# Kernel optimization log

Measured on AMD Instinct MI355X. Metric: run time of the kernel, lower is better.

## Reference

```python
import jax, jax.numpy as jnp
import numpy as np

# Skeleton structure (start, end) connections
REAL_CONNECTIONS = [(0,1),(1,2),(2,3),(3,4),(1,5),(5,6),(6,7),(7,8),(8,9),(8,13),(8,17),(8,21),(8,25),(9,10),(10,11),(11,12),(13,14),(14,15),(15,16),(17,18),(18,19),(19,20),(21,22),(22,23),(23,24),(25,26),(26,27),(27,28),(4,29),(29,30),(29,34),(29,38),(29,42),(29,46),(30,31),(31,32),(32,33),(34,35),(35,36),(36,37),(38,39),(39,40),(40,41),(42,43),(43,44),(44,45),(46,47),(47,48),(48,49)]

def _bone_ranges():
    # dict insertion order matters only for iteration; result is a sum so order-free
    ranges = {(0,1):(0.05,0.15),(1,2):(0.1,0.2),(1,5):(0.1,0.2),(2,3):(0.2,0.35),(3,4):(0.2,0.35),(5,6):(0.2,0.35),(6,7):(0.2,0.35),(4,8):(0.05,0.15),(7,29):(0.05,0.15)}
    for s, e in REAL_CONNECTIONS:
        if 8 <= s < 50 and 8 <= e < 50:
            ranges[(s, e)] = (0.01, 0.08)
    return ranges

_BR = _bone_ranges()
BONE_S = np.array([k[0] for k in _BR], np.int32)
BONE_E = np.array([k[1] for k in _BR], np.int32)
BONE_MIN = np.array([v[0] for v in _BR.values()], np.float32)
BONE_MAX = np.array([v[1] for v in _BR.values()], np.float32)

SYM_L = np.array([8 + i for i in range(21)] + [2, 3, 4], np.int32)
SYM_R = np.array([29 + i for i in range(21)] + [5, 6, 7], np.int32)

ANG_A = np.array([1, 1, 2, 5], np.int32)
ANG_B = np.array([2, 5, 3, 6], np.int32)
ANG_C = np.array([3, 6, 4, 7], np.int32)

CONN_S = np.array([c[0] for c in REAL_CONNECTIONS], np.int32)
CONN_E = np.array([c[1] for c in REAL_CONNECTIONS], np.int32)

DEG = np.float32(180.0 / np.pi)
EPS = np.float32(1e-12)

def _relu(x):
    return jnp.maximum(x, 0.0)

def _normalize(v):
    n = jnp.linalg.norm(v, axis=-1, keepdims=True)
    return v / jnp.maximum(n, EPS)

def setup_inputs() -> dict:
    key = jax.random.key(0)
    k1, k2 = jax.random.split(key)
    B, S, D = 64, 2048, 150
    pred_poses = jax.random.normal(k1, (B, S, D), dtype=jnp.float32)
    target_poses = jax.random.normal(k2, (B, S, D), dtype=jnp.float32)
    return {"pred_poses": pred_poses, "target_poses": target_poses}

def reference(pred_poses, target_poses):
    B, S, _ = pred_poses.shape
    J = pred_poses.reshape(B, S, 50, 3)
    T = target_poses.reshape(B, S, 50, 3)

    # ---- bone length loss (49 constrained bones, one gathered pass) ----
    bv = J[:, :, BONE_E] - J[:, :, BONE_S]                 # [B,S,49,3]
    bl = jnp.linalg.norm(bv, axis=-1)                      # [B,S,49]
    bone_pen = _relu(bl - BONE_MAX) + _relu(BONE_MIN - bl)
    bone_loss = bone_pen.mean()  # == sum over bones of per-bone mean / n_bones

    # ---- joint angle loss (4 triples) ----
    v1 = _normalize(J[:, :, ANG_A] - J[:, :, ANG_B])       # [B,S,4,3]
    v2 = _normalize(J[:, :, ANG_C] - J[:, :, ANG_B])
    cos = jnp.clip(jnp.sum(v1 * v2, axis=-1), -1.0, 1.0)
    deg = jnp.arccos(cos) * DEG
    angle_loss = (_relu(30.0 - deg) + _relu(deg - 150.0)).mean()

    # ---- symmetry loss (24 pairs) ----
    L = J[:, :, SYM_L]                                     # [B,S,24,3]
    R = J[:, :, SYM_R]
    x_sym = jnp.abs(L[..., 0] + R[..., 0])                 # [B,S,24]
    yz_sim = jnp.abs(L[..., 1:] - R[..., 1:]).mean(axis=-1)
    symmetry_loss = (x_sym + yz_sim).mean()

    # ---- temporal consistency ----
    vel = J[:, 1:] - J[:, :-1]                             # [B,S-1,50,3]
    acc = vel[:, 1:] - vel[:, :-1]
    temporal_loss = jnp.linalg.norm(acc, axis=-1).mean() + 0.5 * jnp.linalg.norm(vel, axis=-1).mean()

    # ---- supervised bone-length consistency (all 49 connections) ----
    tb = jnp.linalg.norm(T[:, :, CONN_E] - T[:, :, CONN_S], axis=-1)
    pb = jnp.linalg.norm(J[:, :, CONN_E] - J[:, :, CONN_S], axis=-1)
    supervised_loss = jnp.abs(pb - tb).mean()

    total = (1.0 * bone_loss + 0.5 * angle_loss + 0.3 * symmetry_loss
             + 0.2 * temporal_loss + supervised_loss)
    return bone_loss, angle_loss, symmetry_loss, temporal_loss, supervised_loss, total
```

## Files before the change

kernel.cpp:

```cpp
#include <hip/hip_runtime.h>
#include <math.h>

#define TPB 256
#define CH  16
#define CPB 8

static constexpr int B_     = 64;
static constexpr int S_     = 2048;
static constexpr int TOTAL  = B_ * S_;
static constexpr int NCHUNK = TOTAL / CH;
static constexpr int NBLK   = NCHUNK / CPB;
static constexpr int SAMPB  = 600;
static constexpr int PREDB  = (CH + 2) * SAMPB;
static constexpr int TGTB   = CH * SAMPB;
static constexpr int CHB    = PREDB + TGTB;
static constexpr int BUFB   = 20480;
static constexpr long TOTB  = (long)TOTAL * SAMPB;

__constant__ int US_[51] = {0,1,1,2,3,5,6,4,7,7,4,
    8,8,8,8,8,9,10,11,13,14,
    15,17,18,19,21,22,23,25,26,27,
    29,29,29,29,29,30,31,32,34,35,
    36,38,39,40,42,43,44,46,47,48};
__constant__ int UE_[51] = {1,2,5,3,4,6,7,8,29,8,29,
    9,13,17,21,25,10,11,12,14,15,
    16,18,19,20,22,23,24,26,27,28,
    30,34,38,42,46,31,32,33,35,36,
    37,39,40,41,43,44,45,47,48,49};
__constant__ float UMIN11_[11] = {0.05f,0.1f,0.1f,0.2f,0.2f,0.2f,0.2f,0.05f,0.05f,-1e9f,-1e9f};
__constant__ float UMAX11_[11] = {0.15f,0.2f,0.2f,0.35f,0.35f,0.35f,0.35f,0.15f,0.15f,1e9f,1e9f};
__constant__ float WSUP11_[11] = {1.f,1.f,1.f,1.f,1.f,1.f,1.f,0.f,0.f,1.f,1.f};
__constant__ int SL_[24] = {8,9,10,11,12,13,14,15,16,17,18,19,20,21,22,23,24,25,26,27,28,2,3,4};
__constant__ int SR_[24] = {29,30,31,32,33,34,35,36,37,38,39,40,41,42,43,44,45,46,47,48,49,5,6,7};
__constant__ int AJ_[4] = {1,1,2,5};
__constant__ int BJ_[4] = {2,5,3,6};
__constant__ int CJ_[4] = {3,6,4,7};

struct F3 { float x, y, z; };
__device__ __forceinline__ F3 ld3(const float* p) { return *(const F3*)p; }

typedef const __attribute__((address_space(1))) void* gas_t;
typedef __attribute__((address_space(3))) void* las_t;

__global__ __launch_bounds__(TPB, 4) void pose_main(
    const float* __restrict__ pred, const float* __restrict__ tgt,
    float* __restrict__ part)
{
    __shared__ __align__(16) char LDS[2 * BUFB];

    const int tid = threadIdx.x;
    const int blk = blockIdx.x;
    const int li  = tid & 15;
    const int g   = tid >> 4;
    const int jb  = li * 150;

    int   uS[3], uE[3];
    float uMn[3], uMx[3], uW[3];
    #pragma unroll
    for (int s = 0; s < 3; ++s) {
        const int k = g + 16 * s;
        uS[s] = jb + US_[k] * 3;  uE[s] = jb + UE_[k] * 3;
        uMn[s] = (k < 11) ? UMIN11_[k] : 0.01f;
        uMx[s] = (k < 11) ? UMAX11_[k] : 0.08f;
        uW[s]  = (k < 11) ? WSUP11_[k] : 1.f;
    }
    const int t3 = g - 12;
    const int ke = 48 + (t3 < 0 ? 0 : (t3 > 2 ? 2 : t3));
    const bool e_on = (g >= 12 && g < 15);
    const int   eS = jb + US_[ke] * 3, eE = jb + UE_[ke] * 3;
    const float eMn = e_on ? 0.01f : -1e9f;
    const float eMx = e_on ? 0.08f :  1e9f;
    const float eW  = e_on ? 1.f   :  0.f;
    const int s0L = jb + SL_[g] * 3, s0R = jb + SR_[g] * 3;
    const int k1  = 16 + ((g - 4) & 7);
    const int s1L = jb + SL_[k1] * 3, s1R = jb + SR_[k1] * 3;
    const int aA = jb + AJ_[g & 3] * 3, aB = jb + BJ_[g & 3] * 3, aC = jb + CJ_[g & 3] * 3;
    const int tb0 = jb + 3 * g;
    const int jx  = 48 + ((g - 4) & 1);
    const int tbx = jb + 3 * (jx > 49 ? 49 : jx);
    const bool tex_on = (g == 4 || g == 5);

    float a_bone = 0.f, a_ang = 0.f, a_sym = 0.f, a_vel = 0.f, a_acc = 0.f, a_sup = 0.f;

    auto stage = [&](int cidx, char* lbuf) {
        const long nb = (long)cidx * TGTB;
        const char* pb = (const char*)pred + nb;
        const char* tb = (const char*)tgt  + nb - PREDB;
        const long prem = TOTB - nb - 16;
        char* wdst = lbuf + ((tid >> 6) << 10);
        #pragma unroll
        for (int s = 0; s < 5; ++s) {
            const long o = (long)tid * 16 + s * 4096;
            const char* src = (o < PREDB)
                ? pb + (o > prem ? prem : o)
                : tb + (o > (long)(CHB - 16) ? (long)(CHB - 16) : o);
            __builtin_amdgcn_global_load_lds((gas_t)src, (las_t)(wdst + s * 4096), 16, 0, 0);
        }
    };

    const int c0 = blk * CPB;
    stage(c0, LDS);

    #pragma unroll
    for (int c = 0; c < CPB; ++c) {
        char* curb = LDS + (c & 1) * BUFB;
        char* nxtb = LDS + ((c & 1) ^ 1) * BUFB;
        if (c + 1 < CPB) {
            stage(c0 + c + 1, nxtb);
            asm volatile("s_waitcnt vmcnt(5)" ::: "memory");
        } else {
            asm volatile("s_waitcnt vmcnt(0)" ::: "memory");
        }
        __builtin_amdgcn_s_barrier();
        __builtin_amdgcn_sched_barrier(0);

        const float* Jl = (const float*)curb;
        const float* Tl = Jl + PREDB / 4;
        const int cidx = c0 + c;

        #pragma unroll
        for (int s = 0; s < 3; ++s) {
            const F3 je = ld3(Jl + uE[s]), js = ld3(Jl + uS[s]);
            const float dx = je.x - js.x, dy = je.y - js.y, dz = je.z - js.z;
            const float pb = sqrtf(dx * dx + dy * dy + dz * dz);
            a_bone += fmaxf(pb - uMx[s], 0.f) + fmaxf(uMn[s] - pb, 0.f);
            const F3 te = ld3(Tl + uE[s]), ts = ld3(Tl + uS[s]);
            const float tx = te.x - ts.x, ty = te.y - ts.y, tz = te.z - ts.z;
            const float tb = sqrtf(tx * tx + ty * ty + tz * tz);
            a_sup += uW[s] * fabsf(pb - tb);
        }
        if (tid >= 192) {
            const F3 je = ld3(Jl + eE), js = ld3(Jl + eS);
            const float dx = je.x - js.x, dy = je.y - js.y, dz = je.z - js.z;
            const float pb = sqrtf(dx * dx + dy * dy + dz * dz);
            a_bone += fmaxf(pb - eMx, 0.f) + fmaxf(eMn - pb, 0.f);
            const F3 te = ld3(Tl + eE), ts = ld3(Tl + eS);
            const float tx = te.x - ts.x, ty = te.y - ts.y, tz = te.z - ts.z;
            const float tb = sqrtf(tx * tx + ty * ty + tz * tz);
            a_sup += eW * fabsf(pb - tb);
        }

        {
            const F3 L = ld3(Jl + s0L), R = ld3(Jl + s0R);
            a_sym += fabsf(L.x + R.x) + 0.5f * (fabsf(L.y - R.y) + fabsf(L.z - R.z));
        }
        if (tid >= 64 && tid < 192) {
            const F3 L = ld3(Jl + s1L), R = ld3(Jl + s1R);
            a_sym += fabsf(L.x + R.x) + 0.5f * (fabsf(L.y - R.y) + fabsf(L.z - R.z));
        }

        if (tid < 64) {
            const F3 A = ld3(Jl + aA), Bb = ld3(Jl + aB), C = ld3(Jl + aC);
            const float v1x = A.x - Bb.x, v1y = A.y - Bb.y, v1z = A.z - Bb.z;
            const float v2x = C.x - Bb.x, v2y = C.y - Bb.y, v2z = C.z - Bb.z;
            const float n12 = (v1x*v1x + v1y*v1y + v1z*v1z) * (v2x*v2x + v2y*v2y + v2z*v2z);
            const float inv = __frsqrt_rn(fmaxf(n12, 1e-24f));
            float cosv = (v1x*v2x + v1y*v2y + v1z*v2z) * inv;
            cosv = fminf(fmaxf(cosv, -1.f), 1.f);
            const float deg = acosf(cosv) * 57.29577951308232f;
            a_ang += fmaxf(30.f - deg, 0.f) + fmaxf(deg - 150.f, 0.f);
        }

        {
            const int sidx = ((cidx * CH) & (S_ - 1)) + li;
            const bool v_ok = sidx < S_ - 1;
            const bool a_ok = sidx < S_ - 2;
            const float* tp = Jl + tb0;
            #pragma unroll
            for (int s = 0; s < 3; ++s) {
                const F3 p0 = ld3(tp + 48*s), p1 = ld3(tp + 48*s + 150), p2 = ld3(tp + 48*s + 300);
                if (v_ok) {
                    const float vx = p1.x - p0.x, vy = p1.y - p0.y, vz = p1.z - p0.z;
                    a_vel += sqrtf(vx*vx + vy*vy + vz*vz);
                    if (a_ok) {
                        const float ax = p2.x - 2.f*p1.x + p0.x;
                        const float ay = p2.y - 2.f*p1.y + p0.y;
                        const float az = p2.z - 2.f*p1.z + p0.z;
                        a_acc += sqrtf(ax*ax + ay*ay + az*az);
                    }
                }
            }
            if (tid >= 64 && tid < 128) {
                const float* tq = Jl + tbx;
                const F3 p0 = ld3(tq), p1 = ld3(tq + 150), p2 = ld3(tq + 300);
                if (tex_on && v_ok) {
                    const float vx = p1.x - p0.x, vy = p1.y - p0.y, vz = p1.z - p0.z;
                    a_vel += sqrtf(vx*vx + vy*vy + vz*vz);
                    if (a_ok) {
                        const float ax = p2.x - 2.f*p1.x + p0.x;
                        const float ay = p2.y - 2.f*p1.y + p0.y;
                        const float az = p2.z - 2.f*p1.z + p0.z;
                        a_acc += sqrtf(ax*ax + ay*ay + az*az);
                    }
                }
            }
        }

        asm volatile("" ::: "memory");
        __builtin_amdgcn_s_barrier();
    }

    float vals[6] = {a_bone, a_ang, a_sym, a_vel, a_acc, a_sup};
    #pragma unroll
    for (int k = 0; k < 6; ++k)
        #pragma unroll
        for (int off = 32; off > 0; off >>= 1)
            vals[k] += __shfl_down(vals[k], off, 64);

    float* red = (float*)LDS;
    const int wid = tid >> 6, lane = tid & 63;
    if (lane == 0) {
        #pragma unroll
        for (int k = 0; k < 6; ++k) red[wid * 6 + k] = vals[k];
    }
    __syncthreads();
    if (tid == 0) {
        #pragma unroll
        for (int k = 0; k < 6; ++k)
            part[k * NBLK + blk] = red[k] + red[6 + k] + red[12 + k] + red[18 + k];
    }
}

__global__ __launch_bounds__(256) void pose_reduce(
    const float* __restrict__ part, float* __restrict__ out)
{
    __shared__ float red[4][6];
    const int tid = threadIdx.x;
    float a[6];
    #pragma unroll
    for (int k = 0; k < 6; ++k) {
        float s = 0.f;
        for (int i = tid; i < NBLK; i += 256) s += part[k * NBLK + i];
        a[k] = s;
    }
    #pragma unroll
    for (int k = 0; k < 6; ++k)
        #pragma unroll
        for (int off = 32; off > 0; off >>= 1)
            a[k] += __shfl_down(a[k], off, 64);

    const int wid = tid >> 6, lane = tid & 63;
    if (lane == 0) {
        #pragma unroll
        for (int k = 0; k < 6; ++k) red[wid][k] = a[k];
    }
    __syncthreads();
    if (tid == 0) {
        float t[6];
        #pragma unroll
        for (int k = 0; k < 6; ++k) t[k] = red[0][k] + red[1][k] + red[2][k] + red[3][k];
        const float bone = t[0] * (1.f / ((float)TOTAL * 49.f));
        const float ang  = t[1] * (1.f / ((float)TOTAL * 4.f));
        const float sym  = t[2] * (1.f / ((float)TOTAL * 24.f));
        const float temporal = t[4] * (1.f / ((float)B_ * (float)(S_ - 2) * 50.f))
                             + 0.5f * t[3] * (1.f / ((float)B_ * (float)(S_ - 1) * 50.f));
        const float sup  = t[5] * (1.f / ((float)TOTAL * 49.f));
        out[0] = bone;
        out[1] = ang;
        out[2] = sym;
        out[3] = temporal;
        out[4] = sup;
        out[5] = bone + 0.5f * ang + 0.3f * sym + 0.2f * temporal + sup;
    }
}

extern "C" void kernel_launch(void* const* d_in, const int* in_sizes, int n_in,
                              void* d_out, int out_size, void* d_ws, size_t ws_size,
                              hipStream_t stream)
{
    const float* pred = (const float*)d_in[0];
    const float* tgt  = (const float*)d_in[1];
    float* part = (float*)d_ws;
    pose_main<<<NBLK, TPB, 0, stream>>>(pred, tgt, part);
    pose_reduce<<<1, 256, 0, stream>>>(part, (float*)d_out);
}
```

Baseline: 43.78 us.

## Double block size to 512 threads and redistribute per-thread work

Raises the block to 512 threads (8 waves). Each thread now handles about one bone, symmetry pair and temporal joint instead of up to three, and the staging loads are spread across 8 waves. The per-wave waitcnt values are adjusted to match the uneven load counts. The goal is shorter per-thread serial chains and more latency hiding, at the cost of more idle lanes and heavier barrier synchronisation per block.

```diff
diff --git a/kernel.cpp b/kernel.cpp
--- a/kernel.cpp
+++ b/kernel.cpp
@@ -1,7 +1,7 @@
 #include <hip/hip_runtime.h>
 #include <math.h>
 
-#define TPB 256
+#define TPB 512
 #define CH  16
 #define CPB 8
 
@@ -42,7 +42,7 @@
 typedef const __attribute__((address_space(1))) void* gas_t;
 typedef __attribute__((address_space(3))) void* las_t;
 
-__global__ __launch_bounds__(TPB, 4) void pose_main(
+__global__ __launch_bounds__(TPB, 8) void pose_main(
     const float* __restrict__ pred, const float* __restrict__ tgt,
     float* __restrict__ part)
 {
@@ -54,47 +54,39 @@
     const int g   = tid >> 4;
     const int jb  = li * 150;
 
-    int   uS[3], uE[3];
-    float uMn[3], uMx[3], uW[3];
-    #pragma unroll
-    for (int s = 0; s < 3; ++s) {
-        const int k = g + 16 * s;
-        uS[s] = jb + US_[k] * 3;  uE[s] = jb + UE_[k] * 3;
-        uMn[s] = (k < 11) ? UMIN11_[k] : 0.01f;
-        uMx[s] = (k < 11) ? UMAX11_[k] : 0.08f;
-        uW[s]  = (k < 11) ? WSUP11_[k] : 1.f;
-    }
-    const int t3 = g - 12;
-    const int ke = 48 + (t3 < 0 ? 0 : (t3 > 2 ? 2 : t3));
-    const bool e_on = (g >= 12 && g < 15);
-    const int   eS = jb + US_[ke] * 3, eE = jb + UE_[ke] * 3;
-    const float eMn = e_on ? 0.01f : -1e9f;
-    const float eMx = e_on ? 0.08f :  1e9f;
-    const float eW  = e_on ? 1.f   :  0.f;
-    const int s0L = jb + SL_[g] * 3, s0R = jb + SR_[g] * 3;
-    const int k1  = 16 + ((g - 4) & 7);
-    const int s1L = jb + SL_[k1] * 3, s1R = jb + SR_[k1] * 3;
+    const int   uS0 = jb + US_[g] * 3, uE0 = jb + UE_[g] * 3;
+    const float uMn0 = (g < 11) ? UMIN11_[g] : 0.01f;
+    const float uMx0 = (g < 11) ? UMAX11_[g] : 0.08f;
+    const float uW0  = (g < 11) ? WSUP11_[g] : 1.f;
+    const bool u1_on = (g < 19);
+    const int  k1u   = u1_on ? g + 32 : 50;
+    const int  uS1 = jb + US_[k1u] * 3, uE1 = jb + UE_[k1u] * 3;
+    const bool sy_on = (g < 24);
+    const int  ks  = sy_on ? g : 0;
+    const int  s0L = jb + SL_[ks] * 3, s0R = jb + SR_[ks] * 3;
     const int aA = jb + AJ_[g & 3] * 3, aB = jb + BJ_[g & 3] * 3, aC = jb + CJ_[g & 3] * 3;
-    const int tb0 = jb + 3 * g;
-    const int jx  = 48 + ((g - 4) & 1);
-    const int tbx = jb + 3 * (jx > 49 ? 49 : jx);
-    const bool tex_on = (g == 4 || g == 5);
+    const int  tb0 = jb + 3 * g;
+    const bool t1_on = (g < 18);
 
     float a_bone = 0.f, a_ang = 0.f, a_sym = 0.f, a_vel = 0.f, a_acc = 0.f, a_sup = 0.f;
 
+    const int w      = tid >> 6;
+    const int lane16 = (tid & 63) << 4;
     auto stage = [&](int cidx, char* lbuf) {
         const long nb = (long)cidx * TGTB;
         const char* pb = (const char*)pred + nb;
         const char* tb = (const char*)tgt  + nb - PREDB;
         const long prem = TOTB - nb - 16;
-        char* wdst = lbuf + ((tid >> 6) << 10);
-        #pragma unroll
-        for (int s = 0; s < 5; ++s) {
-            const long o = (long)tid * 16 + s * 4096;
-            const char* src = (o < PREDB)
-                ? pb + (o > prem ? prem : o)
-                : tb + (o > (long)(CHB - 16) ? (long)(CHB - 16) : o);
-            __builtin_amdgcn_global_load_lds((gas_t)src, (las_t)(wdst + s * 4096), 16, 0, 0);
+        #pragma unroll
+        for (int s = 0; s < 3; ++s) {
+            const int slice = w + s * 8;
+            if (slice < 20) {
+                const long o = (long)slice * 1024 + lane16;
+                const char* src = (o < PREDB)
+                    ? pb + (o > prem ? prem : o)
+                    : tb + (o > (long)(CHB - 16) ? (long)(CHB - 16) : o);
+                __builtin_amdgcn_global_load_lds((gas_t)src, (las_t)(lbuf + slice * 1024), 16, 0, 0);
+            }
         }
     };
 
@@ -107,7 +99,8 @@
         char* nxtb = LDS + ((c & 1) ^ 1) * BUFB;
         if (c + 1 < CPB) {
             stage(c0 + c + 1, nxtb);
-            asm volatile("s_waitcnt vmcnt(5)" ::: "memory");
+            if (tid < 256) asm volatile("s_waitcnt vmcnt(3)" ::: "memory");
+            else           asm volatile("s_waitcnt vmcnt(2)" ::: "memory");
         } else {
             asm volatile("s_waitcnt vmcnt(0)" ::: "memory");
         }
@@ -118,34 +111,29 @@
         const float* Tl = Jl + PREDB / 4;
         const int cidx = c0 + c;
 
-        #pragma unroll
-        for (int s = 0; s < 3; ++s) {
-            const F3 je = ld3(Jl + uE[s]), js = ld3(Jl + uS[s]);
+        {
+            const F3 je = ld3(Jl + uE0), js = ld3(Jl + uS0);
             const float dx = je.x - js.x, dy = je.y - js.y, dz = je.z - js.z;
             const float pb = sqrtf(dx * dx + dy * dy + dz * dz);
-            a_bone += fmaxf(pb - uMx[s], 0.f) + fmaxf(uMn[s] - pb, 0.f);
-            const F3 te = ld3(Tl + uE[s]), ts = ld3(Tl + uS[s]);
+            a_bone += fmaxf(pb - uMx0, 0.f) + fmaxf(uMn0 - pb, 0.f);
+            const F3 te = ld3(Tl + uE0), ts = ld3(Tl + uS0);
             const float tx = te.x - ts.x, ty = te.y - ts.y, tz = te.z - ts.z;
             const float tb = sqrtf(tx * tx + ty * ty + tz * tz);
-            a_sup += uW[s] * fabsf(pb - tb);
-        }
-        if (tid >= 192) {
-            const F3 je = ld3(Jl + eE), js = ld3(Jl + eS);
+            a_sup += uW0 * fabsf(pb - tb);
+        }
+        if (u1_on) {
+            const F3 je = ld3(Jl + uE1), js = ld3(Jl + uS1);
             const float dx = je.x - js.x, dy = je.y - js.y, dz = je.z - js.z;
             const float pb = sqrtf(dx * dx + dy * dy + dz * dz);
-            a_bone += fmaxf(pb - eMx, 0.f) + fmaxf(eMn - pb, 0.f);
-            const F3 te = ld3(Tl + eE), ts = ld3(Tl + eS);
+            a_bone += fmaxf(pb - 0.08f, 0.f) + fmaxf(0.01f - pb, 0.f);
+            const F3 te = ld3(Tl + uE1), ts = ld3(Tl + uS1);
             const float tx = te.x - ts.x, ty = te.y - ts.y, tz = te.z - ts.z;
             const float tb = sqrtf(tx * tx + ty * ty + tz * tz);
-            a_sup += eW * fabsf(pb - tb);
-        }
-
-        {
+            a_sup += fabsf(pb - tb);
+        }
+
+        if (sy_on) {
             const F3 L = ld3(Jl + s0L), R = ld3(Jl + s0R);
-            a_sym += fabsf(L.x + R.x) + 0.5f * (fabsf(L.y - R.y) + fabsf(L.z - R.z));
-        }
-        if (tid >= 64 && tid < 192) {
-            const F3 L = ld3(Jl + s1L), R = ld3(Jl + s1R);
             a_sym += fabsf(L.x + R.x) + 0.5f * (fabsf(L.y - R.y) + fabsf(L.z - R.z));
         }
 
@@ -165,10 +153,9 @@
             const int sidx = ((cidx * CH) & (S_ - 1)) + li;
             const bool v_ok = sidx < S_ - 1;
             const bool a_ok = sidx < S_ - 2;
-            const float* tp = Jl + tb0;
-            #pragma unroll
-            for (int s = 0; s < 3; ++s) {
-                const F3 p0 = ld3(tp + 48*s), p1 = ld3(tp + 48*s + 150), p2 = ld3(tp + 48*s + 300);
+            {
+                const float* tp = Jl + tb0;
+                const F3 p0 = ld3(tp), p1 = ld3(tp + 150), p2 = ld3(tp + 300);
                 if (v_ok) {
                     const float vx = p1.x - p0.x, vy = p1.y - p0.y, vz = p1.z - p0.z;
                     a_vel += sqrtf(vx*vx + vy*vy + vz*vz);
@@ -180,10 +167,10 @@
                     }
                 }
             }
-            if (tid >= 64 && tid < 128) {
-                const float* tq = Jl + tbx;
+            if (t1_on) {
+                const float* tq = Jl + tb0 + 96;
                 const F3 p0 = ld3(tq), p1 = ld3(tq + 150), p2 = ld3(tq + 300);
-                if (tex_on && v_ok) {
+                if (v_ok) {
                     const float vx = p1.x - p0.x, vy = p1.y - p0.y, vz = p1.z - p0.z;
                     a_vel += sqrtf(vx*vx + vy*vy + vz*vz);
                     if (a_ok) {
@@ -208,16 +195,20 @@
             vals[k] += __shfl_down(vals[k], off, 64);
 
     float* red = (float*)LDS;
-    const int wid = tid >> 6, lane = tid & 63;
+    const int lane = tid & 63;
     if (lane == 0) {
         #pragma unroll
-        for (int k = 0; k < 6; ++k) red[wid * 6 + k] = vals[k];
+        for (int k = 0; k < 6; ++k) red[w * 6 + k] = vals[k];
     }
     __syncthreads();
     if (tid == 0) {
         #pragma unroll
-        for (int k = 0; k < 6; ++k)
-            part[k * NBLK + blk] = red[k] + red[6 + k] + red[12 + k] + red[18 + k];
+        for (int k = 0; k < 6; ++k) {
+            float s = 0.f;
+            #pragma unroll
+            for (int v = 0; v < 8; ++v) s += red[v * 6 + k];
+            part[k * NBLK + blk] = s;
+        }
     }
 }
 
```

Result: no change. 44.06 us (+0.6%).
